# Kernel optimization log

Hardware: AMD Instinct MI355X
Metric: run time of the kernel (lower is better)

## Reference

```python
import jax, jax.numpy as jnp
import numpy as np

B, S, H, E, K = 2, 1024, 1024, 8, 2
F = 4 * H


def setup_inputs() -> dict:
    key = jax.random.key(0)
    ks = jax.random.split(key, 8)
    std = 0.02
    return {
        "x": jax.random.normal(ks[0], (B, S, H), jnp.float32),
        "gate_w": jax.random.normal(ks[1], (E, H), jnp.float32) * (std / np.sqrt(H)),
        "gate_bias": jnp.zeros((E,), jnp.float32),
        "Wu": jax.random.normal(ks[2], (E, F, H), jnp.float32) * std,
        "bu": jnp.zeros((E, F), jnp.float32),
        "Wd": jax.random.normal(ks[3], (E, H, F), jnp.float32) * std,
        "bd": jnp.zeros((E, H), jnp.float32),
        "sWu": jax.random.normal(ks[4], (F, H), jnp.float32) * std,
        "sbu": jnp.zeros((F,), jnp.float32),
        "sWd": jax.random.normal(ks[5], (H, F), jnp.float32) * std,
        "sbd": jnp.zeros((H,), jnp.float32),
    }


def reference(x, gate_w, gate_bias, Wu, bu, Wd, bd, sWu, sbu, sWd, sbd):
    b, s, h = x.shape
    x_flat = x.reshape(-1, h)                      # [T, H]
    T = x_flat.shape[0]
    # Sigmoid gating + top-k (bias added before sigmoid, as in source)
    scores = jax.nn.sigmoid(x_flat @ gate_w.T + gate_bias)          # [T, E]
    top_scores, top_idx = jax.lax.top_k(scores, K)                  # [T, K]
    top_scores = top_scores / (top_scores.sum(-1, keepdims=True) + 1e-6)
    # Per-token per-expert combine weights (0 for non-selected experts)
    w = jnp.zeros((T, E), x.dtype).at[jnp.arange(T)[:, None], top_idx].add(top_scores)
    # Dense per-expert FFN over all tokens; masked out by w where not routed.
    h1 = jnp.einsum('th,efh->etf', x_flat, Wu) + bu[:, None, :]     # [E, T, F]
    a1 = jax.nn.gelu(h1, approximate=False)
    y = jnp.einsum('etf,ehf->eth', a1, Wd) + bd[:, None, :]         # [E, T, H]
    combined = jnp.einsum('te,eth->th', w, y)                       # [T, H]
    # Shared expert, scaled by 0.1
    sh = jax.nn.gelu(x_flat @ sWu.T + sbu, approximate=False)
    shared = (sh @ sWd.T + sbd) * 0.1
    return (combined + shared).reshape(b, s, h)
```

## Files before the change

### kernel.cpp

```cpp
#include <hip/hip_runtime.h>
#include <cstdint>
#include <cstddef>

#define T_TOK 2048
#define H_DIM 1024
#define E_NUM 8
#define F_DIM 4096
#define NG 9
#define RTOT 6144

typedef unsigned short ushort_t;
typedef __attribute__((ext_vector_type(8))) short bf16x8;
typedef __attribute__((ext_vector_type(4))) float f32x4;

constexpr size_t OFF_TTI = 0;
constexpr size_t OFF_TTW = 16u << 10;
constexpr size_t OFF_CNT = 32u << 10;
constexpr size_t OFF_OFFS = (32u << 10) + 256;
constexpr size_t OFF_RID = 64u << 10;
constexpr size_t OFF_WTS = 96u << 10;
constexpr size_t OFF_XBF = 1u << 20;
constexpr size_t OFF_WUB = 8u << 20;
constexpr size_t OFF_WDB = 80u << 20;
constexpr size_t OFF_A   = 152u << 20;
constexpr size_t OFF_Y   = 200u << 20;

__device__ __forceinline__ ushort_t f2bf(float f) {
  union { float f; unsigned u; } v; v.f = f;
  unsigned r = v.u + 0x7FFFu + ((v.u >> 16) & 1u);
  return (ushort_t)(r >> 16);
}

__device__ __forceinline__ float gelu_exact(float v) {
  return 0.5f * v * (1.0f + erff(v * 0.70710678118654752f));
}

__global__ __launch_bounds__(256) void route_k(const float* __restrict__ x,
                                               const float* __restrict__ gw,
                                               const float* __restrict__ gb,
                                               int* __restrict__ tt_idx,
                                               float* __restrict__ tt_w) {
  const int lane = threadIdx.x & 63;
  const int wid = threadIdx.x >> 6;
  const int t = blockIdx.x * 4 + wid;
  if (t >= T_TOK) return;
  const float* xr = x + (size_t)t * H_DIM;
  float acc[8] = {0.f, 0.f, 0.f, 0.f, 0.f, 0.f, 0.f, 0.f};
  for (int i = 0; i < H_DIM; i += 64) {
    const int k = i + lane;
    const float xv = xr[k];
#pragma unroll
    for (int e = 0; e < 8; ++e) acc[e] = fmaf(xv, gw[e * H_DIM + k], acc[e]);
  }
#pragma unroll
  for (int e = 0; e < 8; ++e) {
    float v = acc[e];
#pragma unroll
    for (int s = 32; s; s >>= 1) v += __shfl_xor(v, s, 64);
    acc[e] = v;
  }
  if (lane == 0) {
    float sc[8];
#pragma unroll
    for (int e = 0; e < 8; ++e) sc[e] = 1.0f / (1.0f + expf(-(acc[e] + gb[e])));
    int i0 = 0;
#pragma unroll
    for (int e = 1; e < 8; ++e) if (sc[e] > sc[i0]) i0 = e;
    int i1 = (i0 == 0) ? 1 : 0;
#pragma unroll
    for (int e = 0; e < 8; ++e) if (e != i0 && sc[e] > sc[i1]) i1 = e;
    const float d = sc[i0] + sc[i1] + 1e-6f;
    tt_idx[2 * t] = i0;
    tt_idx[2 * t + 1] = i1;
    tt_w[2 * t] = sc[i0] / d;
    tt_w[2 * t + 1] = sc[i1] / d;
  }
}

__global__ __launch_bounds__(256) void build_k(const int* __restrict__ tt_idx,
                                               const float* __restrict__ tt_w,
                                               int* __restrict__ counts,
                                               int* __restrict__ offs,
                                               int* __restrict__ rid,
                                               float* __restrict__ wts) {
  __shared__ int cnt[NG];
  __shared__ int cur[NG];
  const int tid = threadIdx.x;
  if (tid < NG) cnt[tid] = 0;
  __syncthreads();
  for (int p = tid; p < 2 * T_TOK; p += 256) atomicAdd(&cnt[tt_idx[p]], 1);
  __syncthreads();
  if (tid == 0) {
    int run = 0;
    for (int e = 0; e < E_NUM; ++e) {
      offs[e] = run;
      counts[e] = cnt[e];
      cur[e] = run;
      run += cnt[e];
    }
    offs[E_NUM] = 2 * T_TOK;
    counts[E_NUM] = T_TOK;
    cur[E_NUM] = 2 * T_TOK;
  }
  __syncthreads();
  for (int p = tid; p < 2 * T_TOK; p += 256) {
    const int e = tt_idx[p];
    const int pos = atomicAdd(&cur[e], 1);
    rid[pos] = ((p >> 1) << 2) | (p & 1);
    wts[pos] = tt_w[p];
  }
  for (int p = tid; p < T_TOK; p += 256) {
    rid[2 * T_TOK + p] = (p << 2) | 2;
    wts[2 * T_TOK + p] = 0.1f;
  }
}

__global__ __launch_bounds__(256) void convert_k(const float* __restrict__ Wu,
                                                 const float* __restrict__ sWu,
                                                 const float* __restrict__ Wd,
                                                 const float* __restrict__ sWd,
                                                 const float* __restrict__ x,
                                                 ushort_t* __restrict__ Wub,
                                                 ushort_t* __restrict__ Wdb,
                                                 ushort_t* __restrict__ Xbf) {
  const long WE = (long)NG * F_DIM * H_DIM;
  const long W8 = (long)8 * F_DIM * H_DIM;
  const long XE = (long)T_TOK * H_DIM;
  const long total = (2 * WE + XE) / 8;
  for (long i = blockIdx.x * 256L + threadIdx.x; i < total; i += (long)gridDim.x * 256L) {
    const long base = i * 8;
    const float* src;
    ushort_t* dst;
    if (base < WE) {
      const long o = base;
      src = (o < W8) ? (Wu + o) : (sWu + (o - W8));
      dst = Wub + o;
    } else if (base < 2 * WE) {
      const long o = base - WE;
      src = (o < W8) ? (Wd + o) : (sWd + (o - W8));
      dst = Wdb + o;
    } else {
      const long o = base - 2 * WE;
      src = x + o;
      dst = Xbf + o;
    }
    const float4 v0 = *(const float4*)src;
    const float4 v1 = *(const float4*)(src + 4);
    bf16x8 r;
    r[0] = (short)f2bf(v0.x); r[1] = (short)f2bf(v0.y);
    r[2] = (short)f2bf(v0.z); r[3] = (short)f2bf(v0.w);
    r[4] = (short)f2bf(v1.x); r[5] = (short)f2bf(v1.y);
    r[6] = (short)f2bf(v1.z); r[7] = (short)f2bf(v1.w);
    *(bf16x8*)dst = r;
  }
}

#define LDS_STRIDE 40
__global__ __launch_bounds__(256) void up_gemm(const ushort_t* __restrict__ Xbf,
                                               const ushort_t* __restrict__ Wub,
                                               const int* __restrict__ counts,
                                               const int* __restrict__ offs,
                                               const int* __restrict__ rid,
                                               const float* __restrict__ wts,
                                               const float* __restrict__ bu,
                                               const float* __restrict__ sbu,
                                               ushort_t* __restrict__ Aout) {
  const int g = blockIdx.y >> 4;
  const int mt = blockIdx.y & 15;
  const int rows = counts[g];
  if (mt * 128 >= rows) return;
  const int off = offs[g];
  const int n0 = blockIdx.x * 128;

  __shared__ ushort_t lA[128 * LDS_STRIDE];
  __shared__ ushort_t lB[128 * LDS_STRIDE];

  const int tid = threadIdx.x;
  const int lane = tid & 63;
  const int wid = tid >> 6;
  const int rs0 = tid >> 2;
  const int cb = (tid & 3) * 8;

  int ig0 = mt * 128 + rs0;        if (ig0 >= rows) ig0 = rows - 1;
  int ig1 = mt * 128 + rs0 + 64;   if (ig1 >= rows) ig1 = rows - 1;
  const ushort_t* srcA0 = Xbf + (size_t)(rid[off + ig0] >> 2) * H_DIM + cb;
  const ushort_t* srcA1 = Xbf + (size_t)(rid[off + ig1] >> 2) * H_DIM + cb;
  const ushort_t* Wg = Wub + (size_t)g * F_DIM * H_DIM;
  const ushort_t* srcB0 = Wg + (size_t)(n0 + rs0) * H_DIM + cb;
  const ushort_t* srcB1 = srcB0 + (size_t)64 * H_DIM;

  f32x4 acc[4][4];
#pragma unroll
  for (int m = 0; m < 4; ++m)
#pragma unroll
    for (int n = 0; n < 4; ++n) acc[m][n] = (f32x4){0.f, 0.f, 0.f, 0.f};

  const int wr = (wid >> 1) * 64;
  const int wc = (wid & 1) * 64;
  const int fr = lane & 15;
  const int fk = (lane >> 4) * 8;

  for (int k0 = 0; k0 < H_DIM; k0 += 32) {
    const bf16x8 va0 = *(const bf16x8*)(srcA0 + k0);
    const bf16x8 va1 = *(const bf16x8*)(srcA1 + k0);
    const bf16x8 vb0 = *(const bf16x8*)(srcB0 + k0);
    const bf16x8 vb1 = *(const bf16x8*)(srcB1 + k0);
    __syncthreads();
    *(bf16x8*)&lA[rs0 * LDS_STRIDE + cb] = va0;
    *(bf16x8*)&lA[(rs0 + 64) * LDS_STRIDE + cb] = va1;
    *(bf16x8*)&lB[rs0 * LDS_STRIDE + cb] = vb0;
    *(bf16x8*)&lB[(rs0 + 64) * LDS_STRIDE + cb] = vb1;
    __syncthreads();
    bf16x8 af[4], bfr[4];
#pragma unroll
    for (int m = 0; m < 4; ++m) af[m] = *(const bf16x8*)&lA[(wr + m * 16 + fr) * LDS_STRIDE + fk];
#pragma unroll
    for (int n = 0; n < 4; ++n) bfr[n] = *(const bf16x8*)&lB[(wc + n * 16 + fr) * LDS_STRIDE + fk];
#pragma unroll
    for (int m = 0; m < 4; ++m)
#pragma unroll
      for (int n = 0; n < 4; ++n)
        acc[m][n] = __builtin_amdgcn_mfma_f32_16x16x32_bf16(af[m], bfr[n], acc[m][n], 0, 0, 0);
  }

  const float* bug = (g < E_NUM) ? (bu + (size_t)g * F_DIM) : sbu;
#pragma unroll
  for (int m = 0; m < 4; ++m) {
#pragma unroll
    for (int q = 0; q < 4; ++q) {
      const int r = wr + m * 16 + (lane >> 4) * 4 + q;
      const int ig = mt * 128 + r;
      if (ig < rows) {
        const float wrow = wts[off + ig];
        const size_t rowbase = (size_t)(off + ig) * F_DIM + n0;
#pragma unroll
        for (int n = 0; n < 4; ++n) {
          const int c = wc + n * 16 + fr;
          const float v = acc[m][n][q] + bug[n0 + c];
          Aout[rowbase + c] = f2bf(gelu_exact(v) * wrow);
        }
      }
    }
  }
}

__global__ __launch_bounds__(256) void down_gemm(const ushort_t* __restrict__ Ain,
                                                 const ushort_t* __restrict__ Wdb,
                                                 const int* __restrict__ counts,
                                                 const int* __restrict__ offs,
                                                 const int* __restrict__ rid,
                                                 float* __restrict__ Y) {
  const int g = blockIdx.y >> 4;
  const int mt = blockIdx.y & 15;
  const int rows = counts[g];
  if (mt * 128 >= rows) return;
  const int off = offs[g];
  const int n0 = blockIdx.x * 128;

  __shared__ ushort_t lA[128 * LDS_STRIDE];
  __shared__ ushort_t lB[128 * LDS_STRIDE];

  const int tid = threadIdx.x;
  const int lane = tid & 63;
  const int wid = tid >> 6;
  const int rs0 = tid >> 2;
  const int cb = (tid & 3) * 8;

  const ushort_t* srcA0 = Ain + (size_t)(off + mt * 128 + rs0) * F_DIM + cb;
  const ushort_t* srcA1 = srcA0 + (size_t)64 * F_DIM;
  const ushort_t* Wg = Wdb + (size_t)g * H_DIM * F_DIM;
  const ushort_t* srcB0 = Wg + (size_t)(n0 + rs0) * F_DIM + cb;
  const ushort_t* srcB1 = srcB0 + (size_t)64 * F_DIM;

  f32x4 acc[4][4];
#pragma unroll
  for (int m = 0; m < 4; ++m)
#pragma unroll
    for (int n = 0; n < 4; ++n) acc[m][n] = (f32x4){0.f, 0.f, 0.f, 0.f};

  const int wr = (wid >> 1) * 64;
  const int wc = (wid & 1) * 64;
  const int fr = lane & 15;
  const int fk = (lane >> 4) * 8;

  for (int k0 = 0; k0 < F_DIM; k0 += 32) {
    const bf16x8 va0 = *(const bf16x8*)(srcA0 + k0);
    const bf16x8 va1 = *(const bf16x8*)(srcA1 + k0);
    const bf16x8 vb0 = *(const bf16x8*)(srcB0 + k0);
    const bf16x8 vb1 = *(const bf16x8*)(srcB1 + k0);
    __syncthreads();
    *(bf16x8*)&lA[rs0 * LDS_STRIDE + cb] = va0;
    *(bf16x8*)&lA[(rs0 + 64) * LDS_STRIDE + cb] = va1;
    *(bf16x8*)&lB[rs0 * LDS_STRIDE + cb] = vb0;
    *(bf16x8*)&lB[(rs0 + 64) * LDS_STRIDE + cb] = vb1;
    __syncthreads();
    bf16x8 af[4], bfr[4];
#pragma unroll
    for (int m = 0; m < 4; ++m) af[m] = *(const bf16x8*)&lA[(wr + m * 16 + fr) * LDS_STRIDE + fk];
#pragma unroll
    for (int n = 0; n < 4; ++n) bfr[n] = *(const bf16x8*)&lB[(wc + n * 16 + fr) * LDS_STRIDE + fk];
#pragma unroll
    for (int m = 0; m < 4; ++m)
#pragma unroll
      for (int n = 0; n < 4; ++n)
        acc[m][n] = __builtin_amdgcn_mfma_f32_16x16x32_bf16(af[m], bfr[n], acc[m][n], 0, 0, 0);
  }

#pragma unroll
  for (int m = 0; m < 4; ++m) {
#pragma unroll
    for (int q = 0; q < 4; ++q) {
      const int r = wr + m * 16 + (lane >> 4) * 4 + q;
      const int ig = mt * 128 + r;
      if (ig < rows) {
        const int rv = rid[off + ig];
        const size_t yb = ((size_t)(rv >> 2) * 3 + (rv & 3)) * H_DIM + n0;
#pragma unroll
        for (int n = 0; n < 4; ++n) {
          const int c = wc + n * 16 + fr;
          Y[yb + c] = acc[m][n][q];
        }
      }
    }
  }
}

__global__ __launch_bounds__(256) void combine_k(const float* __restrict__ Y,
                                                 const int* __restrict__ tt_idx,
                                                 const float* __restrict__ tt_w,
                                                 const float* __restrict__ bd,
                                                 const float* __restrict__ sbd,
                                                 float* __restrict__ out) {
  const int t = blockIdx.x;
  const int h = threadIdx.x * 4;
  const int e0 = tt_idx[2 * t];
  const int e1 = tt_idx[2 * t + 1];
  const float w0 = tt_w[2 * t];
  const float w1 = tt_w[2 * t + 1];
  const float4 y0 = *(const float4*)(Y + ((size_t)t * 3 + 0) * H_DIM + h);
  const float4 y1 = *(const float4*)(Y + ((size_t)t * 3 + 1) * H_DIM + h);
  const float4 y2 = *(const float4*)(Y + ((size_t)t * 3 + 2) * H_DIM + h);
  const float4 b0 = *(const float4*)(bd + (size_t)e0 * H_DIM + h);
  const float4 b1 = *(const float4*)(bd + (size_t)e1 * H_DIM + h);
  const float4 bs = *(const float4*)(sbd + h);
  float4 o;
  o.x = y0.x + y1.x + y2.x + w0 * b0.x + w1 * b1.x + 0.1f * bs.x;
  o.y = y0.y + y1.y + y2.y + w0 * b0.y + w1 * b1.y + 0.1f * bs.y;
  o.z = y0.z + y1.z + y2.z + w0 * b0.z + w1 * b1.z + 0.1f * bs.z;
  o.w = y0.w + y1.w + y2.w + w0 * b0.w + w1 * b1.w + 0.1f * bs.w;
  *(float4*)(out + (size_t)t * H_DIM + h) = o;
}

extern "C" void kernel_launch(void* const* d_in, const int* in_sizes, int n_in,
                              void* d_out, int out_size, void* d_ws, size_t ws_size,
                              hipStream_t stream) {
  (void)in_sizes; (void)n_in; (void)out_size; (void)ws_size;
  const float* x = (const float*)d_in[0];
  const float* gate_w = (const float*)d_in[1];
  const float* gate_b = (const float*)d_in[2];
  const float* Wu = (const float*)d_in[3];
  const float* bu = (const float*)d_in[4];
  const float* Wd = (const float*)d_in[5];
  const float* bd = (const float*)d_in[6];
  const float* sWu = (const float*)d_in[7];
  const float* sbu = (const float*)d_in[8];
  const float* sWd = (const float*)d_in[9];
  const float* sbd = (const float*)d_in[10];
  float* out = (float*)d_out;

  char* ws = (char*)d_ws;
  int* tt_idx = (int*)(ws + OFF_TTI);
  float* tt_w = (float*)(ws + OFF_TTW);
  int* counts = (int*)(ws + OFF_CNT);
  int* offs = (int*)(ws + OFF_OFFS);
  int* rid = (int*)(ws + OFF_RID);
  float* wts = (float*)(ws + OFF_WTS);
  ushort_t* Xbf = (ushort_t*)(ws + OFF_XBF);
  ushort_t* Wub = (ushort_t*)(ws + OFF_WUB);
  ushort_t* Wdb = (ushort_t*)(ws + OFF_WDB);
  ushort_t* A = (ushort_t*)(ws + OFF_A);
  float* Y = (float*)(ws + OFF_Y);

  hipLaunchKernelGGL(route_k, dim3(T_TOK / 4), dim3(256), 0, stream,
                     x, gate_w, gate_b, tt_idx, tt_w);
  hipLaunchKernelGGL(build_k, dim3(1), dim3(256), 0, stream,
                     tt_idx, tt_w, counts, offs, rid, wts);
  hipLaunchKernelGGL(convert_k, dim3(4096), dim3(256), 0, stream,
                     Wu, sWu, Wd, sWd, x, Wub, Wdb, Xbf);
  hipLaunchKernelGGL(up_gemm, dim3(F_DIM / 128, NG * 16), dim3(256), 0, stream,
                     Xbf, Wub, counts, offs, rid, wts, bu, sbu, A);
  hipLaunchKernelGGL(down_gemm, dim3(H_DIM / 128, NG * 16), dim3(256), 0, stream,
                     A, Wdb, counts, offs, rid, Y);
  hipLaunchKernelGGL(combine_k, dim3(T_TOK), dim3(256), 0, stream,
                     Y, tt_idx, tt_w, bd, sbd, out);
}
```

Baseline: 649.0 us.

## Use direct global-to-LDS loads with swizzle, split-K down GEMM with atomic combine

Both grouped GEMMs now stage tiles through global_load_lds into an XOR-swizzled 64-wide LDS layout. This removes the register round-trip and the padded layout, and the K step doubles to 64. The down GEMM is split four ways along K and accumulates straight into the output with float atomics, after a new bias_init kernel writes the bias terms. That removes the Y buffer and the combine kernel, and the split gives four times as many blocks for parallelism. In exchange it adds atomic contention and makes the summation order nondeterministic.

```diff
diff --git a/kernel.cpp b/kernel.cpp
--- a/kernel.cpp
+++ b/kernel.cpp
@@ -7,11 +7,13 @@
 #define E_NUM 8
 #define F_DIM 4096
 #define NG 9
-#define RTOT 6144
 
 typedef unsigned short ushort_t;
 typedef __attribute__((ext_vector_type(8))) short bf16x8;
 typedef __attribute__((ext_vector_type(4))) float f32x4;
+typedef unsigned int u32;
+typedef u32 __attribute__((address_space(3))) lds_u32;
+typedef u32 __attribute__((address_space(1))) glob_u32;
 
 constexpr size_t OFF_TTI = 0;
 constexpr size_t OFF_TTW = 16u << 10;
@@ -23,7 +25,6 @@
 constexpr size_t OFF_WUB = 8u << 20;
 constexpr size_t OFF_WDB = 80u << 20;
 constexpr size_t OFF_A   = 152u << 20;
-constexpr size_t OFF_Y   = 200u << 20;
 
 __device__ __forceinline__ ushort_t f2bf(float f) {
   union { float f; unsigned u; } v; v.f = f;
@@ -33,6 +34,10 @@
 
 __device__ __forceinline__ float gelu_exact(float v) {
   return 0.5f * v * (1.0f + erff(v * 0.70710678118654752f));
+}
+
+__device__ __forceinline__ void gll16(const ushort_t* g, ushort_t* l) {
+  __builtin_amdgcn_global_load_lds((glob_u32*)(g), (lds_u32*)(l), 16, 0, 0);
 }
 
 __global__ __launch_bounds__(256) void route_k(const float* __restrict__ x,
@@ -155,7 +160,28 @@
   }
 }
 
-#define LDS_STRIDE 40
+__global__ __launch_bounds__(256) void bias_init(const int* __restrict__ tt_idx,
+                                                 const float* __restrict__ tt_w,
+                                                 const float* __restrict__ bd,
+                                                 const float* __restrict__ sbd,
+                                                 float* __restrict__ out) {
+  const int t = blockIdx.x;
+  const int h = threadIdx.x * 4;
+  const int e0 = tt_idx[2 * t];
+  const int e1 = tt_idx[2 * t + 1];
+  const float w0 = tt_w[2 * t];
+  const float w1 = tt_w[2 * t + 1];
+  const float4 b0 = *(const float4*)(bd + (size_t)e0 * H_DIM + h);
+  const float4 b1 = *(const float4*)(bd + (size_t)e1 * H_DIM + h);
+  const float4 bs = *(const float4*)(sbd + h);
+  float4 o;
+  o.x = w0 * b0.x + w1 * b1.x + 0.1f * bs.x;
+  o.y = w0 * b0.y + w1 * b1.y + 0.1f * bs.y;
+  o.z = w0 * b0.z + w1 * b1.z + 0.1f * bs.z;
+  o.w = w0 * b0.w + w1 * b1.w + 0.1f * bs.w;
+  *(float4*)(out + (size_t)t * H_DIM + h) = o;
+}
+
 __global__ __launch_bounds__(256) void up_gemm(const ushort_t* __restrict__ Xbf,
                                                const ushort_t* __restrict__ Wub,
                                                const int* __restrict__ counts,
@@ -172,22 +198,26 @@
   const int off = offs[g];
   const int n0 = blockIdx.x * 128;
 
-  __shared__ ushort_t lA[128 * LDS_STRIDE];
-  __shared__ ushort_t lB[128 * LDS_STRIDE];
+  __shared__ ushort_t lA[128 * 64];
+  __shared__ ushort_t lB[128 * 64];
 
   const int tid = threadIdx.x;
   const int lane = tid & 63;
   const int wid = tid >> 6;
-  const int rs0 = tid >> 2;
-  const int cb = (tid & 3) * 8;
-
-  int ig0 = mt * 128 + rs0;        if (ig0 >= rows) ig0 = rows - 1;
-  int ig1 = mt * 128 + rs0 + 64;   if (ig1 >= rows) ig1 = rows - 1;
-  const ushort_t* srcA0 = Xbf + (size_t)(rid[off + ig0] >> 2) * H_DIM + cb;
-  const ushort_t* srcA1 = Xbf + (size_t)(rid[off + ig1] >> 2) * H_DIM + cb;
+  const int sr = lane >> 3;
+  const int swz = ((lane & 7) ^ sr) << 3;
+
   const ushort_t* Wg = Wub + (size_t)g * F_DIM * H_DIM;
-  const ushort_t* srcB0 = Wg + (size_t)(n0 + rs0) * H_DIM + cb;
-  const ushort_t* srcB1 = srcB0 + (size_t)64 * H_DIM;
+  const ushort_t* pA[4];
+  const ushort_t* pB[4];
+#pragma unroll
+  for (int i = 0; i < 4; ++i) {
+    const int rA = (wid * 4 + i) * 8 + sr;
+    int ig = mt * 128 + rA;
+    if (ig >= rows) ig = rows - 1;
+    pA[i] = Xbf + (size_t)(rid[off + ig] >> 2) * H_DIM + swz;
+    pB[i] = Wg + (size_t)(n0 + rA) * H_DIM + swz;
+  }
 
   f32x4 acc[4][4];
 #pragma unroll
@@ -198,29 +228,36 @@
   const int wr = (wid >> 1) * 64;
   const int wc = (wid & 1) * 64;
   const int fr = lane & 15;
-  const int fk = (lane >> 4) * 8;
-
-  for (int k0 = 0; k0 < H_DIM; k0 += 32) {
-    const bf16x8 va0 = *(const bf16x8*)(srcA0 + k0);
-    const bf16x8 va1 = *(const bf16x8*)(srcA1 + k0);
-    const bf16x8 vb0 = *(const bf16x8*)(srcB0 + k0);
-    const bf16x8 vb1 = *(const bf16x8*)(srcB1 + k0);
+  const int hi = lane >> 4;
+
+  for (int k0 = 0; k0 < H_DIM; k0 += 64) {
     __syncthreads();
-    *(bf16x8*)&lA[rs0 * LDS_STRIDE + cb] = va0;
-    *(bf16x8*)&lA[(rs0 + 64) * LDS_STRIDE + cb] = va1;
-    *(bf16x8*)&lB[rs0 * LDS_STRIDE + cb] = vb0;
-    *(bf16x8*)&lB[(rs0 + 64) * LDS_STRIDE + cb] = vb1;
+#pragma unroll
+    for (int i = 0; i < 4; ++i) {
+      gll16(pA[i] + k0, &lA[(wid * 4 + i) * 512]);
+      gll16(pB[i] + k0, &lB[(wid * 4 + i) * 512]);
+    }
     __syncthreads();
-    bf16x8 af[4], bfr[4];
-#pragma unroll
-    for (int m = 0; m < 4; ++m) af[m] = *(const bf16x8*)&lA[(wr + m * 16 + fr) * LDS_STRIDE + fk];
-#pragma unroll
-    for (int n = 0; n < 4; ++n) bfr[n] = *(const bf16x8*)&lB[(wc + n * 16 + fr) * LDS_STRIDE + fk];
-#pragma unroll
-    for (int m = 0; m < 4; ++m)
-#pragma unroll
-      for (int n = 0; n < 4; ++n)
-        acc[m][n] = __builtin_amdgcn_mfma_f32_16x16x32_bf16(af[m], bfr[n], acc[m][n], 0, 0, 0);
+#pragma unroll
+    for (int ks = 0; ks < 2; ++ks) {
+      const int cc = ks * 4 + hi;
+      bf16x8 af[4], bv[4];
+#pragma unroll
+      for (int m = 0; m < 4; ++m) {
+        const int r = wr + m * 16 + fr;
+        af[m] = *(const bf16x8*)&lA[r * 64 + ((cc ^ (r & 7)) << 3)];
+      }
+#pragma unroll
+      for (int n = 0; n < 4; ++n) {
+        const int r = wc + n * 16 + fr;
+        bv[n] = *(const bf16x8*)&lB[r * 64 + ((cc ^ (r & 7)) << 3)];
+      }
+#pragma unroll
+      for (int m = 0; m < 4; ++m)
+#pragma unroll
+        for (int n = 0; n < 4; ++n)
+          acc[m][n] = __builtin_amdgcn_mfma_f32_16x16x32_bf16(af[m], bv[n], acc[m][n], 0, 0, 0);
+    }
   }
 
   const float* bug = (g < E_NUM) ? (bu + (size_t)g * F_DIM) : sbu;
@@ -228,7 +265,7 @@
   for (int m = 0; m < 4; ++m) {
 #pragma unroll
     for (int q = 0; q < 4; ++q) {
-      const int r = wr + m * 16 + (lane >> 4) * 4 + q;
+      const int r = wr + m * 16 + hi * 4 + q;
       const int ig = mt * 128 + r;
       if (ig < rows) {
         const float wrow = wts[off + ig];
@@ -249,28 +286,33 @@
                                                  const int* __restrict__ counts,
                                                  const int* __restrict__ offs,
                                                  const int* __restrict__ rid,
-                                                 float* __restrict__ Y) {
+                                                 float* __restrict__ out) {
   const int g = blockIdx.y >> 4;
   const int mt = blockIdx.y & 15;
   const int rows = counts[g];
   if (mt * 128 >= rows) return;
   const int off = offs[g];
   const int n0 = blockIdx.x * 128;
-
-  __shared__ ushort_t lA[128 * LDS_STRIDE];
-  __shared__ ushort_t lB[128 * LDS_STRIDE];
+  const int kbase = blockIdx.z * 1024;
+
+  __shared__ ushort_t lA[128 * 64];
+  __shared__ ushort_t lB[128 * 64];
 
   const int tid = threadIdx.x;
   const int lane = tid & 63;
   const int wid = tid >> 6;
-  const int rs0 = tid >> 2;
-  const int cb = (tid & 3) * 8;
-
-  const ushort_t* srcA0 = Ain + (size_t)(off + mt * 128 + rs0) * F_DIM + cb;
-  const ushort_t* srcA1 = srcA0 + (size_t)64 * F_DIM;
+  const int sr = lane >> 3;
+  const int swz = ((lane & 7) ^ sr) << 3;
+
   const ushort_t* Wg = Wdb + (size_t)g * H_DIM * F_DIM;
-  const ushort_t* srcB0 = Wg + (size_t)(n0 + rs0) * F_DIM + cb;
-  const ushort_t* srcB1 = srcB0 + (size_t)64 * F_DIM;
+  const ushort_t* pA[4];
+  const ushort_t* pB[4];
+#pragma unroll
+  for (int i = 0; i < 4; ++i) {
+    const int rA = (wid * 4 + i) * 8 + sr;
+    pA[i] = Ain + (size_t)(off + mt * 128 + rA) * F_DIM + kbase + swz;
+    pB[i] = Wg + (size_t)(n0 + rA) * F_DIM + kbase + swz;
+  }
 
   f32x4 acc[4][4];
 #pragma unroll
@@ -281,74 +323,55 @@
   const int wr = (wid >> 1) * 64;
   const int wc = (wid & 1) * 64;
   const int fr = lane & 15;
-  const int fk = (lane >> 4) * 8;
-
-  for (int k0 = 0; k0 < F_DIM; k0 += 32) {
-    const bf16x8 va0 = *(const bf16x8*)(srcA0 + k0);
-    const bf16x8 va1 = *(const bf16x8*)(srcA1 + k0);
-    const bf16x8 vb0 = *(const bf16x8*)(srcB0 + k0);
-    const bf16x8 vb1 = *(const bf16x8*)(srcB1 + k0);
+  const int hi = lane >> 4;
+
+  for (int k0 = 0; k0 < 1024; k0 += 64) {
     __syncthreads();
-    *(bf16x8*)&lA[rs0 * LDS_STRIDE + cb] = va0;
-    *(bf16x8*)&lA[(rs0 + 64) * LDS_STRIDE + cb] = va1;
-    *(bf16x8*)&lB[rs0 * LDS_STRIDE + cb] = vb0;
-    *(bf16x8*)&lB[(rs0 + 64) * LDS_STRIDE + cb] = vb1;
+#pragma unroll
+    for (int i = 0; i < 4; ++i) {
+      gll16(pA[i] + k0, &lA[(wid * 4 + i) * 512]);
+      gll16(pB[i] + k0, &lB[(wid * 4 + i) * 512]);
+    }
     __syncthreads();
-    bf16x8 af[4], bfr[4];
-#pragma unroll
-    for (int m = 0; m < 4; ++m) af[m] = *(const bf16x8*)&lA[(wr + m * 16 + fr) * LDS_STRIDE + fk];
-#pragma unroll
-    for (int n = 0; n < 4; ++n) bfr[n] = *(const bf16x8*)&lB[(wc + n * 16 + fr) * LDS_STRIDE + fk];
-#pragma unroll
-    for (int m = 0; m < 4; ++m)
-#pragma unroll
-      for (int n = 0; n < 4; ++n)
-        acc[m][n] = __builtin_amdgcn_mfma_f32_16x16x32_bf16(af[m], bfr[n], acc[m][n], 0, 0, 0);
+#pragma unroll
+    for (int ks = 0; ks < 2; ++ks) {
+      const int cc = ks * 4 + hi;
+      bf16x8 af[4], bv[4];
+#pragma unroll
+      for (int m = 0; m < 4; ++m) {
+        const int r = wr + m * 16 + fr;
+        af[m] = *(const bf16x8*)&lA[r * 64 + ((cc ^ (r & 7)) << 3)];
+      }
+#pragma unroll
+      for (int n = 0; n < 4; ++n) {
+        const int r = wc + n * 16 + fr;
+        bv[n] = *(const bf16x8*)&lB[r * 64 + ((cc ^ (r & 7)) << 3)];
+      }
+#pragma unroll
+      for (int m = 0; m < 4; ++m)
+#pragma unroll
+        for (int n = 0; n < 4; ++n)
+          acc[m][n] = __builtin_amdgcn_mfma_f32_16x16x32_bf16(af[m], bv[n], acc[m][n], 0, 0, 0);
+    }
   }
 
 #pragma unroll
   for (int m = 0; m < 4; ++m) {
 #pragma unroll
     for (int q = 0; q < 4; ++q) {
-      const int r = wr + m * 16 + (lane >> 4) * 4 + q;
+      const int r = wr + m * 16 + hi * 4 + q;
       const int ig = mt * 128 + r;
       if (ig < rows) {
         const int rv = rid[off + ig];
-        const size_t yb = ((size_t)(rv >> 2) * 3 + (rv & 3)) * H_DIM + n0;
+        float* orow = out + (size_t)(rv >> 2) * H_DIM + n0;
 #pragma unroll
         for (int n = 0; n < 4; ++n) {
           const int c = wc + n * 16 + fr;
-          Y[yb + c] = acc[m][n][q];
+          unsafeAtomicAdd(&orow[c], acc[m][n][q]);
         }
       }
     }
   }
-}
-
-__global__ __launch_bounds__(256) void combine_k(const float* __restrict__ Y,
-                                                 const int* __restrict__ tt_idx,
-                                                 const float* __restrict__ tt_w,
-                                                 const float* __restrict__ bd,
-                                                 const float* __restrict__ sbd,
-                                                 float* __restrict__ out) {
-  const int t = blockIdx.x;
-  const int h = threadIdx.x * 4;
-  const int e0 = tt_idx[2 * t];
-  const int e1 = tt_idx[2 * t + 1];
-  const float w0 = tt_w[2 * t];
-  const float w1 = tt_w[2 * t + 1];
-  const float4 y0 = *(const float4*)(Y + ((size_t)t * 3 + 0) * H_DIM + h);
-  const float4 y1 = *(const float4*)(Y + ((size_t)t * 3 + 1) * H_DIM + h);
-  const float4 y2 = *(const float4*)(Y + ((size_t)t * 3 + 2) * H_DIM + h);
-  const float4 b0 = *(const float4*)(bd + (size_t)e0 * H_DIM + h);
-  const float4 b1 = *(const float4*)(bd + (size_t)e1 * H_DIM + h);
-  const float4 bs = *(const float4*)(sbd + h);
-  float4 o;
-  o.x = y0.x + y1.x + y2.x + w0 * b0.x + w1 * b1.x + 0.1f * bs.x;
-  o.y = y0.y + y1.y + y2.y + w0 * b0.y + w1 * b1.y + 0.1f * bs.y;
-  o.z = y0.z + y1.z + y2.z + w0 * b0.z + w1 * b1.z + 0.1f * bs.z;
-  o.w = y0.w + y1.w + y2.w + w0 * b0.w + w1 * b1.w + 0.1f * bs.w;
-  *(float4*)(out + (size_t)t * H_DIM + h) = o;
 }
 
 extern "C" void kernel_launch(void* const* d_in, const int* in_sizes, int n_in,
@@ -379,18 +402,17 @@
   ushort_t* Wub = (ushort_t*)(ws + OFF_WUB);
   ushort_t* Wdb = (ushort_t*)(ws + OFF_WDB);
   ushort_t* A = (ushort_t*)(ws + OFF_A);
-  float* Y = (float*)(ws + OFF_Y);
 
   hipLaunchKernelGGL(route_k, dim3(T_TOK / 4), dim3(256), 0, stream,
                      x, gate_w, gate_b, tt_idx, tt_w);
   hipLaunchKernelGGL(build_k, dim3(1), dim3(256), 0, stream,
                      tt_idx, tt_w, counts, offs, rid, wts);
+  hipLaunchKernelGGL(bias_init, dim3(T_TOK), dim3(256), 0, stream,
+                     tt_idx, tt_w, bd, sbd, out);
   hipLaunchKernelGGL(convert_k, dim3(4096), dim3(256), 0, stream,
                      Wu, sWu, Wd, sWd, x, Wub, Wdb, Xbf);
   hipLaunchKernelGGL(up_gemm, dim3(F_DIM / 128, NG * 16), dim3(256), 0, stream,
                      Xbf, Wub, counts, offs, rid, wts, bu, sbu, A);
-  hipLaunchKernelGGL(down_gemm, dim3(H_DIM / 128, NG * 16), dim3(256), 0, stream,
-                     A, Wdb, counts, offs, rid, Y);
-  hipLaunchKernelGGL(combine_k, dim3(T_TOK), dim3(256), 0, stream,
-                     Y, tt_idx, tt_w, bd, sbd, out);
-}
+  hipLaunchKernelGGL(down_gemm, dim3(H_DIM / 128, NG * 16, 4), dim3(256), 0, stream,
+                     A, Wdb, counts, offs, rid, out);
+}
```

After: 633.6 us. 2.4% less time.
